# Kernel tuning notes

Hardware: AMD Instinct MI355X
Metric: run time of the kernel (lower is better)

Reference implementation:

```python
import jax, jax.numpy as jnp
import numpy as np

BS, N, IN_DIM, OUT_DIM = 16, 2048, 32, 64
CHEB_K, E_NODE, T_D = 3, 10, 8
EMBED = E_NODE + T_D  # 18, matches weights_pool dim 0
TOPK = 10


def setup_inputs() -> dict:
    key = jax.random.key(0)
    ks = jax.random.split(key, 7)
    return {
        "x": jax.random.normal(ks[0], (BS, N, IN_DIM), jnp.float32),
        "node_emb": jax.random.normal(ks[1], (N, E_NODE), jnp.float32),
        "t": jax.random.normal(ks[2], (BS, T_D), jnp.float32),
        "n_t": jax.random.normal(ks[3], (BS, T_D), jnp.float32),
        "p": jax.random.normal(ks[4], (BS, 1, 1), jnp.float32),
        "weights_pool": jax.random.normal(ks[5], (EMBED, CHEB_K, IN_DIM, OUT_DIM), jnp.float32) * 0.1,
        "bias_pool": jax.random.normal(ks[6], (EMBED, OUT_DIM), jnp.float32) * 0.1,
    }


def reference(x, node_emb, t, n_t, p, weights_pool, bias_pool):
    bs, n, _ = x.shape
    # static adjacency from node embeddings, broadcast over batch: [bs, N, N]
    a = (node_emb @ node_emb.T)[None, :, :]
    # temporal scalar correction: bmm([bs,1,td],[bs,td,1]) -> [bs,1,1]
    a_t = jnp.einsum('bd,bd->b', n_t, t)[:, None, None]
    _a = a + a_t
    # period branch: scaled relu adjacency, then dynamic topK sparsify
    pre = jax.nn.relu((1.0 + 0.3 * jax.nn.sigmoid(p)) * _a)  # [bs, N, N]
    # topK tie-break noise (torch.rand_like * 0.01); deterministic key here
    noise = jax.random.uniform(jax.random.key(42), pre.shape, jnp.float32) * 0.01
    _, idx = jax.lax.top_k(pre + noise, TOPK)  # idx: [bs, N, TOPK]
    mask = jnp.zeros_like(pre).at[
        jnp.arange(bs)[:, None, None], jnp.arange(n)[None, :, None], idx
    ].set(1.0)
    # masked entries stay 0 (not -inf) before softmax, as in the original
    A = jax.nn.softmax(pre * mask, axis=2)
    # Chebyshev polynomial supports: T0=I, T1=A, Tk = 2*A@T(k-1) - T(k-2)
    I = jnp.broadcast_to(jnp.eye(n, dtype=x.dtype), (bs, n, n))
    supports = [I, A]
    for _ in range(2, CHEB_K):
        supports.append(2.0 * (A @ supports[-1]) - supports[-2])
    S = jnp.stack(supports, axis=1)  # [bs, K, N, N]
    # node-adaptive embedding: cat(node_emb, n_t) -> [bs, N, EMBED]
    ne = jnp.concatenate(
        [jnp.broadcast_to(node_emb[None], (bs, n, E_NODE)),
         jnp.broadcast_to(n_t[:, None, :], (bs, n, T_D))], axis=-1)
    # graph conv features: [bs, N, K, in]
    x_g = jnp.einsum('bknm,bmc->bnkc', S, x)
    bias = ne @ bias_pool  # [bs, N, out]
    # fused per-node dynamic-weight contraction:
    # original: W = einsum(bnd,dkio->bnkio); out = einsum(bnki,bnkio->bno)
    out = jnp.einsum('bnki,bnd,dkio->bno', x_g, ne, weights_pool) + bias
    return out
```

## Files before the change

kernel.cpp:

```cpp
#include <hip/hip_runtime.h>
#include <hip/hip_bf16.h>


constexpr int BS = 16, NN_ = 2048, CIN = 32, OUT = 64, TK = 10;
constexpr int ROWS = BS * NN_;

__device__ __forceinline__ void tf2x32(unsigned x0, unsigned x1,
                                       unsigned& o0, unsigned& o1) {
  const unsigned k0 = 0u, k1 = 42u;
  const unsigned ks2 = k0 ^ k1 ^ 0x1BD11BDAu;
#define TF_R(rot) { x0 += x1; x1 = (x1 << rot) | (x1 >> (32 - rot)); x1 ^= x0; }
  x0 += k0; x1 += k1;
  TF_R(13) TF_R(15) TF_R(26) TF_R(6)
  x0 += k1; x1 += ks2 + 1u;
  TF_R(17) TF_R(29) TF_R(16) TF_R(24)
  x0 += ks2; x1 += k0 + 2u;
  TF_R(13) TF_R(15) TF_R(26) TF_R(6)
  x0 += k0; x1 += k1 + 3u;
  TF_R(17) TF_R(29) TF_R(16) TF_R(24)
  x0 += k1; x1 += ks2 + 4u;
  TF_R(13) TF_R(15) TF_R(26) TF_R(6)
  x0 += ks2; x1 += k0 + 5u;
#undef TF_R
  o0 = x0; o1 = x1;
}

__device__ __forceinline__ float noise_val(unsigned flat) {
  unsigned o0, o1; tf2x32(0u, flat, o0, o1);
  unsigned bits = o0 ^ o1;
  float u = __uint_as_float((bits >> 9) | 0x3f800000u) - 1.0f;
  return 0.01f * u;
}

__global__ __launch_bounds__(256) void k_pre(const float* __restrict__ ne,
                                             const float* __restrict__ n_t,
                                             const float* __restrict__ wp,
                                             const float* __restrict__ x,
                                             float* __restrict__ Wn,
                                             float* __restrict__ Wt,
                                             double* __restrict__ csxD) {
  const int bid = blockIdx.x;
  __shared__ float neS[16][10];
  __shared__ double red[8][32];

  if (bid < 768) {
    const int ng = bid / 6, sg = bid % 6;
    const int slot = sg * 256 + threadIdx.x;
    const int ki = slot >> 4, o4 = slot & 15;

    if (threadIdx.x < 160)
      neS[threadIdx.x / 10][threadIdx.x % 10] =
          ne[(ng * 16 + threadIdx.x / 10) * 10 + threadIdx.x % 10];

    const float4* wp4 = (const float4*)wp;
    float4 w[10];
    #pragma unroll
    for (int d = 0; d < 10; ++d) w[d] = wp4[(d * 96 + ki) * 16 + o4];
    __syncthreads();

    float4* Wn4 = (float4*)Wn;
    #pragma unroll 4
    for (int nn = 0; nn < 16; ++nn) {
      float4 acc = {0.f, 0.f, 0.f, 0.f};
      #pragma unroll
      for (int d = 0; d < 10; ++d) {
        float e = neS[nn][d];
        acc.x = fmaf(e, w[d].x, acc.x); acc.y = fmaf(e, w[d].y, acc.y);
        acc.z = fmaf(e, w[d].z, acc.z); acc.w = fmaf(e, w[d].w, acc.w);
      }
      Wn4[((size_t)(ng * 16 + nn) * 96 + ki) * 16 + o4] = acc;
    }
  } else if (bid < 864) {
    int gid = (bid - 768) * 256 + threadIdx.x;
    int b = gid / 1536, rem = gid % 1536, ki = rem >> 4, o4 = rem & 15;
    const float4* wp4 = (const float4*)wp;
    float4 acc = {0.f, 0.f, 0.f, 0.f};
    #pragma unroll
    for (int d = 0; d < 8; ++d) {
      float e = n_t[b * 8 + d];
      float4 w = wp4[((10 + d) * 96 + ki) * 16 + o4];
      acc.x = fmaf(e, w.x, acc.x); acc.y = fmaf(e, w.y, acc.y);
      acc.z = fmaf(e, w.z, acc.z); acc.w = fmaf(e, w.w, acc.w);
    }
    ((float4*)Wt)[(b * 96 + ki) * 16 + o4] = acc;
  } else {
    const int bb = bid - 864;
    const int b = bb >> 4, ch = bb & 15;
    const int c = threadIdx.x & 31, g = threadIdx.x >> 5;
    double acc = 0.0;
    for (int m = ch * 128 + g; m < ch * 128 + 128; m += 8)
      acc += (double)x[(((b << 11) + m) << 5) + c];
    red[g][c] = acc;
    __syncthreads();
    if (g == 0) {
      double s2 = red[0][c];
      #pragma unroll
      for (int i = 1; i < 8; ++i) s2 += red[i][c];
      atomicAdd(&csxD[(b << 5) + c], s2);
    }
  }
}

__global__ __launch_bounds__(256, 4) void k_topk(const float* __restrict__ ne,
                                                 const float* __restrict__ t,
                                                 const float* __restrict__ n_t,
                                                 const float* __restrict__ p,
                                                 const float* __restrict__ x,
                                                 const double* __restrict__ csxD,
                                                 float* __restrict__ cinv,
                                                 int* __restrict__ idxb,
                                                 float* __restrict__ wgt,
                                                 float* __restrict__ Y1,
                                                 float* __restrict__ csy_part) {
  const int n = blockIdx.x;
  const int warp = threadIdx.x >> 6, lane = threadIdx.x & 63;

  __shared__ float rowS[2048];
  __shared__ float candA[4][128];
  __shared__ int   candM[4][128];
  __shared__ unsigned long long keyS[4][128];
  __shared__ int   winI[16][10];
  __shared__ float winW[16][10];
  __shared__ float ciS[16];

  {
    float ner[10];
    #pragma unroll
    for (int d = 0; d < 10; ++d) ner[d] = ne[n * 10 + d];
    #pragma unroll
    for (int g2 = 0; g2 < 2; ++g2) {
      const int m0 = g2 * 1024 + threadIdx.x * 4;
      const float4* nf = (const float4*)(ne + (size_t)m0 * 10);
      float acc4[4] = {0.f, 0.f, 0.f, 0.f};
      #pragma unroll
      for (int i = 0; i < 10; ++i) {
        float4 q = nf[i];
        #pragma unroll
        for (int j = 0; j < 4; ++j) {
          const int e = i * 4 + j;
          const int rr = e / 10, d = e % 10;
          acc4[rr] = fmaf(ner[d], (&q.x)[j], acc4[rr]);
        }
      }
      *(float4*)&rowS[m0] = make_float4(acc4[0], acc4[1], acc4[2], acc4[3]);
    }
  }
  __syncthreads();

  float lm = -3.4e38f;
  #pragma unroll
  for (int j = 0; j < 8; ++j) {
    float4 f = ((const float4*)rowS)[j * 64 + lane];
    lm = fmaxf(lm, fmaxf(fmaxf(f.x, f.y), fmaxf(f.z, f.w)));
  }
  float last = 3.4e38f;
  for (int rd = 0; rd < 11; ++rd) {
    float x2 = (lm < last) ? lm : -3.4e38f;
    #pragma unroll
    for (int off = 32; off > 0; off >>= 1) x2 = fmaxf(x2, __shfl_xor(x2, off));
    last = x2;
  }
  const float T = last - 0.0101f;

  int cnt = 0;
  #pragma unroll
  for (int slot = 0; slot < 32; ++slot) {
    float v = rowS[(slot >> 2) * 256 + lane * 4 + (slot & 3)];
    bool c = (v >= T);
    unsigned long long mk = __ballot(c);
    if (c) {
      int pos = cnt + __popcll(mk & ((1ull << lane) - 1ull));
      if (pos < 128) {
        candA[warp][pos] = v;
        candM[warp][pos] = ((slot >> 2) << 8) + (lane << 2) + (slot & 3);
      }
    }
    cnt += (int)__popcll(mk);
  }
  const int C = cnt < 128 ? cnt : 128;

  if (C <= 32) {
    const int h = lane >> 5, j = lane & 31;
    for (int pair = 0; pair < 2; ++pair) {
      const int b = warp * 4 + pair * 2 + h;
      const int r = (b << 11) | n;

      float at = 0.f;
      #pragma unroll
      for (int d = 0; d < 8; ++d) at = fmaf(n_t[b * 8 + d], t[b * 8 + d], at);
      const float s = 1.0f + 0.3f * (1.0f / (1.0f + expf(-p[b])));

      const bool act = (j < C);
      float pre = 0.f; int mj = 0;
      unsigned long long kk = 0ull;
      if (act) {
        float aj = candA[warp][j]; mj = candM[warp][j];
        pre = fmaxf(s * (aj + at), 0.f);
        float key = pre + noise_val((unsigned)r * 2048u + (unsigned)mj);
        kk = ((unsigned long long)__float_as_uint(key) << 32) |
             (unsigned)(2047 - mj);
      }
      keyS[warp][lane] = kk;

      int rank = 0;
      for (int j2 = 0; j2 < C; ++j2) {
        unsigned long long kj = keyS[warp][h * 32 + j2];
        rank += (kj > kk) ? 1 : 0;
      }
      const bool win = act && (rank < 10);

      float e = win ? expf(pre) : 0.f;
      float sum = e;
      #pragma unroll
      for (int off = 16; off > 0; off >>= 1) sum += __shfl_xor(sum, off);
      const float ci = 1.0f / (2038.0f + sum);

      unsigned long long mask = __ballot(win);
      unsigned mh = (unsigned)(mask >> (h * 32));
      if (win) {
        int pos = __popc(mh & ((1u << j) - 1u));
        idxb[r * 10 + pos] = mj;
        wgt[r * 10 + pos] = (e - 1.0f) * ci;
        winI[b][pos] = mj;
        winW[b][pos] = (e - 1.0f) * ci;
      }
      if (j == 0) { cinv[r] = ci; ciS[b] = ci; }
    }
  } else {
    const bool two = (C > 64);
    float a0c = 0.f, a1c = 0.f; int m0c = 0, m1c = 0;
    if (lane < C) { a0c = candA[warp][lane]; m0c = candM[warp][lane]; }
    if (two && lane + 64 < C) {
      a1c = candA[warp][lane + 64]; m1c = candM[warp][lane + 64];
    }
    for (int bi = 0; bi < 4; ++bi) {
      const int b = warp * 4 + bi;
      const int r = (b << 11) | n;

      float at = 0.f;
      #pragma unroll
      for (int d = 0; d < 8; ++d) at = fmaf(n_t[b * 8 + d], t[b * 8 + d], at);
      const float s = 1.0f + 0.3f * (1.0f / (1.0f + expf(-p[b])));

      float pre0 = fmaxf(s * (a0c + at), 0.f);
      unsigned long long k0 = 0ull;
      if (lane < C) {
        float key0 = pre0 + noise_val((unsigned)r * 2048u + (unsigned)m0c);
        k0 = ((unsigned long long)__float_as_uint(key0) << 32) |
             (unsigned)(2047 - m0c);
        keyS[warp][lane] = k0;
      }
      float pre1 = 0.f;
      unsigned long long k1 = 0ull;
      if (two) {
        if (lane + 64 < C) {
          pre1 = fmaxf(s * (a1c + at), 0.f);
          float key1 = pre1 + noise_val((unsigned)r * 2048u + (unsigned)m1c);
          k1 = ((unsigned long long)__float_as_uint(key1) << 32) |
               (unsigned)(2047 - m1c);
        }
        keyS[warp][lane + 64] = k1;
      }

      int rank0 = 0, rank1 = 0;
      for (int j2 = 0; j2 < C; ++j2) {
        unsigned long long kj = keyS[warp][j2];
        rank0 += (kj > k0) ? 1 : 0;
        if (two) rank1 += (kj > k1) ? 1 : 0;
      }
      bool w0 = (lane < C) && (rank0 < 10);
      bool w1 = two && (lane + 64 < C) && (rank1 < 10);

      float e0 = w0 ? expf(pre0) : 0.f;
      float e1 = w1 ? expf(pre1) : 0.f;
      float sum = e0 + e1;
      #pragma unroll
      for (int off = 32; off > 0; off >>= 1) sum += __shfl_xor(sum, off);
      const float ci = 1.0f / (2038.0f + sum);

      unsigned long long mk0 = __ballot(w0);
      if (w0) {
        int pos = __popcll(mk0 & ((1ull << lane) - 1ull));
        idxb[r * 10 + pos] = m0c;
        wgt[r * 10 + pos] = (e0 - 1.0f) * ci;
        winI[b][pos] = m0c;
        winW[b][pos] = (e0 - 1.0f) * ci;
      }
      if (two) {
        unsigned long long mk1 = __ballot(w1);
        int base = __popcll(mk0);
        if (w1) {
          int pos = base + __popcll(mk1 & ((1ull << lane) - 1ull));
          idxb[r * 10 + pos] = m1c;
          wgt[r * 10 + pos] = (e1 - 1.0f) * ci;
          winI[b][pos] = m1c;
          winW[b][pos] = (e1 - 1.0f) * ci;
        }
      }
      if (lane == 0) { cinv[r] = ci; ciS[b] = ci; }
    }
  }

  #pragma unroll
  for (int pass = 0; pass < 2; ++pass) {
    const int bi2 = pass * 2 + (lane >> 5);
    const int b = warp * 4 + bi2;
    const int c = lane & 31;
    const int r = (b << 11) | n;
    float acc = ciS[b] * (float)csxD[(b << 5) + c];
    #pragma unroll
    for (int j = 0; j < 10; ++j) {
      int m = winI[b][j];
      float w = winW[b][j];
      acc = fmaf(w, x[(((b << 11) + m) << 5) + c], acc);
    }
    Y1[(size_t)r * 32 + c] = acc;
    atomicAdd(&csy_part[((n & 7) << 9) + (b << 5) + c], acc);
  }
}

__global__ __launch_bounds__(256) void k_v(const float* __restrict__ x,
                                           const float* __restrict__ Y1,
                                           const float* __restrict__ cinv,
                                           const int* __restrict__ idxb,
                                           const float* __restrict__ wgt,
                                           const float* __restrict__ csy_part,
                                           float* __restrict__ V) {
  int gid = blockIdx.x * 256 + threadIdx.x;
  int r = gid >> 5, c = gid & 31, b = r >> 11;
  float cs = 0.f;
  #pragma unroll
  for (int k = 0; k < 8; ++k) cs += csy_part[(k << 9) + (b << 5) + c];
  float y2 = cinv[r] * cs;
  #pragma unroll
  for (int j = 0; j < 10; ++j)
    y2 = fmaf(wgt[r * 10 + j], Y1[(((b << 11) + idxb[r * 10 + j]) << 5) + c], y2);
  float xv = x[gid], y1v = Y1[gid];
  V[r * 96 + c] = xv;
  V[r * 96 + 32 + c] = y1v;
  V[r * 96 + 64 + c] = 2.f * y2 - xv;
}

__global__ __launch_bounds__(256) void k_outn(const float* __restrict__ ne,
                                              const float* __restrict__ n_t,
                                              const float* __restrict__ Wn,
                                              const float* __restrict__ bp,
                                              const float* __restrict__ V,
                                              float* __restrict__ out) {
  const int n = blockIdx.x;
  __shared__ float Vs[16][100];
  __shared__ float bNs[64];

  for (int e = threadIdx.x; e < 384; e += 256) {
    int b = e / 24, j4 = e % 24;
    float4 f = *(const float4*)&V[((size_t)(b << 11) + n) * 96 + j4 * 4];
    *(float4*)&Vs[b][j4 * 4] = f;
  }
  if (threadIdx.x < 64) {
    float acc = 0.f;
    #pragma unroll
    for (int d = 0; d < 10; ++d)
      acc = fmaf(ne[n * 10 + d], bp[d * 64 + threadIdx.x], acc);
    bNs[threadIdx.x] = acc;
  }
  __syncthreads();

  const int b = threadIdx.x >> 4, og = threadIdx.x & 15;
  const float4* Wr = (const float4*)(Wn + (size_t)n * 6144);

  float4 acc = {0.f, 0.f, 0.f, 0.f};
  #pragma unroll 4
  for (int ki = 0; ki < 96; ++ki) {
    float4 wv = Wr[ki * 16 + og];
    float v = Vs[b][ki];
    acc.x = fmaf(v, wv.x, acc.x); acc.y = fmaf(v, wv.y, acc.y);
    acc.z = fmaf(v, wv.z, acc.z); acc.w = fmaf(v, wv.w, acc.w);
  }

  float4 res;
  #pragma unroll
  for (int q = 0; q < 4; ++q) {
    int o = og * 4 + q;
    float bT = 0.f;
    #pragma unroll
    for (int d = 0; d < 8; ++d)
      bT = fmaf(n_t[b * 8 + d], bp[(10 + d) * 64 + o], bT);
    (&res.x)[q] = (&acc.x)[q] + bNs[o] + bT;
  }
  *(float4*)&out[((size_t)(b << 11) + n) * 64 + og * 4] = res;
}

__global__ __launch_bounds__(512) void k_outt(const float* __restrict__ WtG,
                                              const float* __restrict__ V,
                                              float* __restrict__ out) {
  const int b = blockIdx.x >> 5, tile = blockIdx.x & 31;
  __shared__ float Wt[96][64];
  {
    const float4* src = (const float4*)(WtG + (size_t)b * 6144);
    float4* dst = (float4*)Wt;
    for (int e = threadIdx.x; e < 1536; e += 512) dst[e] = src[e];
  }
  __syncthreads();
  const int wave = threadIdx.x >> 6, lane = threadIdx.x & 63;
  const int og = lane & 15, rg = lane >> 4;
  const int r0 = tile * 64 + wave * 8 + rg * 2;

  float acc[2][4] = {};
  for (int ki4 = 0; ki4 < 24; ++ki4) {
    float4 vv[2];
    #pragma unroll
    for (int i = 0; i < 2; ++i)
      vv[i] = *(const float4*)&V[(size_t)((b << 11) + r0 + i) * 96 + ki4 * 4];
    #pragma unroll
    for (int t2 = 0; t2 < 4; ++t2) {
      float4 wv = *(const float4*)&Wt[ki4 * 4 + t2][og * 4];
      #pragma unroll
      for (int i = 0; i < 2; ++i) {
        float vi = (t2 == 0) ? vv[i].x : (t2 == 1) ? vv[i].y
                 : (t2 == 2) ? vv[i].z : vv[i].w;
        acc[i][0] = fmaf(vi, wv.x, acc[i][0]);
        acc[i][1] = fmaf(vi, wv.y, acc[i][1]);
        acc[i][2] = fmaf(vi, wv.z, acc[i][2]);
        acc[i][3] = fmaf(vi, wv.w, acc[i][3]);
      }
    }
  }
  #pragma unroll
  for (int i = 0; i < 2; ++i) {
    size_t oidx = (size_t)((b << 11) + r0 + i) * 64 + og * 4;
    float4 cur = *(float4*)&out[oidx];
    cur.x += acc[i][0]; cur.y += acc[i][1];
    cur.z += acc[i][2]; cur.w += acc[i][3];
    *(float4*)&out[oidx] = cur;
  }
}

extern "C" void kernel_launch(void* const* d_in, const int* in_sizes, int n_in,
                              void* d_out, int out_size, void* d_ws, size_t ws_size,
                              hipStream_t stream) {
  const float* x   = (const float*)d_in[0];
  const float* ne  = (const float*)d_in[1];
  const float* t   = (const float*)d_in[2];
  const float* n_t = (const float*)d_in[3];
  const float* p   = (const float*)d_in[4];
  const float* wp  = (const float*)d_in[5];
  const float* bp  = (const float*)d_in[6];
  float* out = (float*)d_out;
  float* ws = (float*)d_ws;
  (void)in_sizes; (void)n_in; (void)out_size; (void)ws_size;

  float* cinv     = ws;
  int*   idxb     = (int*)(cinv + 32768);
  float* wgt      = (float*)(idxb + 327680);
  double* csxD    = (double*)(wgt + 327680);
  float* csy_part = (float*)(csxD + 512);
  float* Y1       = csy_part + 4096;
  float* V        = Y1 + 1048576;
  float* Wt       = V + 3145728;
  float* Wn       = Wt + 98304;

  hipMemsetAsync(csxD, 0, 512 * 8 + 4096 * 4, stream);

  k_pre  <<<1120, 256, 0, stream>>>(ne, n_t, wp, x, Wn, Wt, csxD);
  k_topk <<<2048, 256, 0, stream>>>(ne, t, n_t, p, x, csxD,
                                    cinv, idxb, wgt, Y1, csy_part);
  k_v    <<<4096, 256, 0, stream>>>(x, Y1, cinv, idxb, wgt, csy_part, V);
  k_outn <<<2048, 256, 0, stream>>>(ne, n_t, Wn, bp, V, out);
  k_outt <<<512, 512, 0, stream>>>(Wt, V, out);
}
```

Before: 173.8 us.

## Move weight precompute into topk kernel and fuse V build into node output

The Wn/Wt dynamic-weight precompute moves out of the first kernel into extra leading blocks of the topk kernel, leaving a small column-sum kernel ahead of it. The separate V-construction kernel is folded into the per-node output kernel, which now builds V rows directly in shared memory while still writing V for the later Wt kernel. This removes one launch and the global round trip of V before the node contraction, and lets the weight precompute overlap with topk work. In exchange the topk kernel grid grows with heterogeneous blocks, and the node output kernel performs gathers whose access pattern is less coalesced than the old dedicated kernel.

```diff
diff --git a/kernel.cpp b/kernel.cpp
--- a/kernel.cpp
+++ b/kernel.cpp
@@ -32,72 +32,21 @@
   return 0.01f * u;
 }
 
-__global__ __launch_bounds__(256) void k_pre(const float* __restrict__ ne,
-                                             const float* __restrict__ n_t,
-                                             const float* __restrict__ wp,
-                                             const float* __restrict__ x,
-                                             float* __restrict__ Wn,
-                                             float* __restrict__ Wt,
+__global__ __launch_bounds__(256) void k_csx(const float* __restrict__ x,
                                              double* __restrict__ csxD) {
-  const int bid = blockIdx.x;
-  __shared__ float neS[16][10];
+  const int b = blockIdx.x >> 4, ch = blockIdx.x & 15;
+  const int c = threadIdx.x & 31, g = threadIdx.x >> 5;
   __shared__ double red[8][32];
-
-  if (bid < 768) {
-    const int ng = bid / 6, sg = bid % 6;
-    const int slot = sg * 256 + threadIdx.x;
-    const int ki = slot >> 4, o4 = slot & 15;
-
-    if (threadIdx.x < 160)
-      neS[threadIdx.x / 10][threadIdx.x % 10] =
-          ne[(ng * 16 + threadIdx.x / 10) * 10 + threadIdx.x % 10];
-
-    const float4* wp4 = (const float4*)wp;
-    float4 w[10];
-    #pragma unroll
-    for (int d = 0; d < 10; ++d) w[d] = wp4[(d * 96 + ki) * 16 + o4];
-    __syncthreads();
-
-    float4* Wn4 = (float4*)Wn;
-    #pragma unroll 4
-    for (int nn = 0; nn < 16; ++nn) {
-      float4 acc = {0.f, 0.f, 0.f, 0.f};
-      #pragma unroll
-      for (int d = 0; d < 10; ++d) {
-        float e = neS[nn][d];
-        acc.x = fmaf(e, w[d].x, acc.x); acc.y = fmaf(e, w[d].y, acc.y);
-        acc.z = fmaf(e, w[d].z, acc.z); acc.w = fmaf(e, w[d].w, acc.w);
-      }
-      Wn4[((size_t)(ng * 16 + nn) * 96 + ki) * 16 + o4] = acc;
-    }
-  } else if (bid < 864) {
-    int gid = (bid - 768) * 256 + threadIdx.x;
-    int b = gid / 1536, rem = gid % 1536, ki = rem >> 4, o4 = rem & 15;
-    const float4* wp4 = (const float4*)wp;
-    float4 acc = {0.f, 0.f, 0.f, 0.f};
-    #pragma unroll
-    for (int d = 0; d < 8; ++d) {
-      float e = n_t[b * 8 + d];
-      float4 w = wp4[((10 + d) * 96 + ki) * 16 + o4];
-      acc.x = fmaf(e, w.x, acc.x); acc.y = fmaf(e, w.y, acc.y);
-      acc.z = fmaf(e, w.z, acc.z); acc.w = fmaf(e, w.w, acc.w);
-    }
-    ((float4*)Wt)[(b * 96 + ki) * 16 + o4] = acc;
-  } else {
-    const int bb = bid - 864;
-    const int b = bb >> 4, ch = bb & 15;
-    const int c = threadIdx.x & 31, g = threadIdx.x >> 5;
-    double acc = 0.0;
-    for (int m = ch * 128 + g; m < ch * 128 + 128; m += 8)
-      acc += (double)x[(((b << 11) + m) << 5) + c];
-    red[g][c] = acc;
-    __syncthreads();
-    if (g == 0) {
-      double s2 = red[0][c];
-      #pragma unroll
-      for (int i = 1; i < 8; ++i) s2 += red[i][c];
-      atomicAdd(&csxD[(b << 5) + c], s2);
-    }
+  double acc = 0.0;
+  for (int m = ch * 128 + g; m < ch * 128 + 128; m += 8)
+    acc += (double)x[(((b << 11) + m) << 5) + c];
+  red[g][c] = acc;
+  __syncthreads();
+  if (g == 0) {
+    double s2 = red[0][c];
+    #pragma unroll
+    for (int i = 1; i < 8; ++i) s2 += red[i][c];
+    atomicAdd(&csxD[(b << 5) + c], s2);
   }
 }
 
@@ -107,12 +56,15 @@
                                                  const float* __restrict__ p,
                                                  const float* __restrict__ x,
                                                  const double* __restrict__ csxD,
+                                                 const float* __restrict__ wp,
                                                  float* __restrict__ cinv,
                                                  int* __restrict__ idxb,
                                                  float* __restrict__ wgt,
                                                  float* __restrict__ Y1,
-                                                 float* __restrict__ csy_part) {
-  const int n = blockIdx.x;
+                                                 float* __restrict__ csy_part,
+                                                 float* __restrict__ Wn,
+                                                 float* __restrict__ Wt) {
+  const int bid = blockIdx.x;
   const int warp = threadIdx.x >> 6, lane = threadIdx.x & 63;
 
   __shared__ float rowS[2048];
@@ -122,6 +74,53 @@
   __shared__ int   winI[16][10];
   __shared__ float winW[16][10];
   __shared__ float ciS[16];
+
+  if (bid < 768) {
+    float* neS = rowS;
+    const int ng = bid / 6, sg = bid % 6;
+    const int slot = sg * 256 + threadIdx.x;
+    const int ki = slot >> 4, o4 = slot & 15;
+
+    if (threadIdx.x < 160)
+      neS[threadIdx.x] = ne[ng * 160 + threadIdx.x];
+
+    const float4* wp4 = (const float4*)wp;
+    float4 w[10];
+    #pragma unroll
+    for (int d = 0; d < 10; ++d) w[d] = wp4[(d * 96 + ki) * 16 + o4];
+    __syncthreads();
+
+    float4* Wn4 = (float4*)Wn;
+    #pragma unroll 4
+    for (int nn = 0; nn < 16; ++nn) {
+      float4 acc = {0.f, 0.f, 0.f, 0.f};
+      #pragma unroll
+      for (int d = 0; d < 10; ++d) {
+        float e = neS[nn * 10 + d];
+        acc.x = fmaf(e, w[d].x, acc.x); acc.y = fmaf(e, w[d].y, acc.y);
+        acc.z = fmaf(e, w[d].z, acc.z); acc.w = fmaf(e, w[d].w, acc.w);
+      }
+      Wn4[((size_t)(ng * 16 + nn) * 96 + ki) * 16 + o4] = acc;
+    }
+    return;
+  }
+  if (bid < 864) {
+    int gid = (bid - 768) * 256 + threadIdx.x;
+    int b = gid / 1536, rem = gid % 1536, ki = rem >> 4, o4 = rem & 15;
+    const float4* wp4 = (const float4*)wp;
+    float4 acc = {0.f, 0.f, 0.f, 0.f};
+    #pragma unroll
+    for (int d = 0; d < 8; ++d) {
+      float e = n_t[b * 8 + d];
+      float4 w = wp4[((10 + d) * 96 + ki) * 16 + o4];
+      acc.x = fmaf(e, w.x, acc.x); acc.y = fmaf(e, w.y, acc.y);
+      acc.z = fmaf(e, w.z, acc.z); acc.w = fmaf(e, w.w, acc.w);
+    }
+    ((float4*)Wt)[(b * 96 + ki) * 16 + o4] = acc;
+    return;
+  }
+
+  const int n = bid - 864;
 
   {
     float ner[10];
@@ -319,42 +318,50 @@
   }
 }
 
-__global__ __launch_bounds__(256) void k_v(const float* __restrict__ x,
-                                           const float* __restrict__ Y1,
-                                           const float* __restrict__ cinv,
-                                           const int* __restrict__ idxb,
-                                           const float* __restrict__ wgt,
-                                           const float* __restrict__ csy_part,
-                                           float* __restrict__ V) {
-  int gid = blockIdx.x * 256 + threadIdx.x;
-  int r = gid >> 5, c = gid & 31, b = r >> 11;
-  float cs = 0.f;
-  #pragma unroll
-  for (int k = 0; k < 8; ++k) cs += csy_part[(k << 9) + (b << 5) + c];
-  float y2 = cinv[r] * cs;
-  #pragma unroll
-  for (int j = 0; j < 10; ++j)
-    y2 = fmaf(wgt[r * 10 + j], Y1[(((b << 11) + idxb[r * 10 + j]) << 5) + c], y2);
-  float xv = x[gid], y1v = Y1[gid];
-  V[r * 96 + c] = xv;
-  V[r * 96 + 32 + c] = y1v;
-  V[r * 96 + 64 + c] = 2.f * y2 - xv;
-}
-
-__global__ __launch_bounds__(256) void k_outn(const float* __restrict__ ne,
-                                              const float* __restrict__ n_t,
-                                              const float* __restrict__ Wn,
-                                              const float* __restrict__ bp,
-                                              const float* __restrict__ V,
-                                              float* __restrict__ out) {
+__global__ __launch_bounds__(256) void k_nodeout(const float* __restrict__ ne,
+                                                 const float* __restrict__ n_t,
+                                                 const float* __restrict__ Wn,
+                                                 const float* __restrict__ bp,
+                                                 const float* __restrict__ x,
+                                                 const float* __restrict__ Y1,
+                                                 const float* __restrict__ cinv,
+                                                 const int* __restrict__ idxb,
+                                                 const float* __restrict__ wgt,
+                                                 const float* __restrict__ csy_part,
+                                                 float* __restrict__ V,
+                                                 float* __restrict__ out) {
   const int n = blockIdx.x;
   __shared__ float Vs[16][100];
   __shared__ float bNs[64];
 
-  for (int e = threadIdx.x; e < 384; e += 256) {
-    int b = e / 24, j4 = e % 24;
-    float4 f = *(const float4*)&V[((size_t)(b << 11) + n) * 96 + j4 * 4];
-    *(float4*)&Vs[b][j4 * 4] = f;
+  {
+    const int b = threadIdx.x >> 4, c2 = threadIdx.x & 15;
+    const int r = (b << 11) | n;
+    const float ci = cinv[r];
+    int mj[10]; float wj[10];
+    #pragma unroll
+    for (int j = 0; j < 10; ++j) {
+      mj[j] = idxb[r * 10 + j];
+      wj[j] = wgt[r * 10 + j];
+    }
+    #pragma unroll
+    for (int cc = 0; cc < 2; ++cc) {
+      const int c = c2 + cc * 16;
+      float cs = 0.f;
+      #pragma unroll
+      for (int k = 0; k < 8; ++k) cs += csy_part[(k << 9) + (b << 5) + c];
+      float y2 = ci * cs;
+      #pragma unroll
+      for (int j = 0; j < 10; ++j)
+        y2 = fmaf(wj[j], Y1[(((b << 11) + mj[j]) << 5) + c], y2);
+      float xv = x[((size_t)r << 5) + c];
+      float y1v = Y1[((size_t)r << 5) + c];
+      float ch2 = 2.f * y2 - xv;
+      Vs[b][c] = xv; Vs[b][32 + c] = y1v; Vs[b][64 + c] = ch2;
+      V[(size_t)r * 96 + c] = xv;
+      V[(size_t)r * 96 + 32 + c] = y1v;
+      V[(size_t)r * 96 + 64 + c] = ch2;
+    }
   }
   if (threadIdx.x < 64) {
     float acc = 0.f;
@@ -461,10 +468,10 @@
 
   hipMemsetAsync(csxD, 0, 512 * 8 + 4096 * 4, stream);
 
-  k_pre  <<<1120, 256, 0, stream>>>(ne, n_t, wp, x, Wn, Wt, csxD);
-  k_topk <<<2048, 256, 0, stream>>>(ne, t, n_t, p, x, csxD,
-                                    cinv, idxb, wgt, Y1, csy_part);
-  k_v    <<<4096, 256, 0, stream>>>(x, Y1, cinv, idxb, wgt, csy_part, V);
-  k_outn <<<2048, 256, 0, stream>>>(ne, n_t, Wn, bp, V, out);
-  k_outt <<<512, 512, 0, stream>>>(Wt, V, out);
-}
+  k_csx    <<<256, 256, 0, stream>>>(x, csxD);
+  k_topk   <<<2912, 256, 0, stream>>>(ne, t, n_t, p, x, csxD, wp,
+                                      cinv, idxb, wgt, Y1, csy_part, Wn, Wt);
+  k_nodeout<<<2048, 256, 0, stream>>>(ne, n_t, Wn, bp, x, Y1,
+                                      cinv, idxb, wgt, csy_part, V, out);
+  k_outt   <<<512, 512, 0, stream>>>(Wt, V, out);
+}
```

Result: no change. 171.2 us (-1.5%).
